# Kernel tuning notes

Measured on AMD Instinct MI355X. Metric: run time of the kernel, lower is better.

## Reference

```python
import jax, jax.numpy as jnp
import numpy as np

N, E, G = 50000, 800000, 16
NODE, HID, OUT, HEADS = 128, 64, 128, 3
NEG_SLOPE = 0.2

def setup_inputs() -> dict:
    key = jax.random.key(0)
    ks = jax.random.split(key, 12)
    h = jax.random.normal(ks[0], (N, NODE), jnp.float32)
    z = jax.random.normal(ks[1], (G, OUT), jnp.float32)
    src = jax.random.randint(ks[2], (E,), 0, N, jnp.int32)
    dst = jax.random.randint(ks[3], (E,), 0, N, jnp.int32)
    graph_id = jnp.sort(jax.random.randint(ks[4], (N,), 0, G, jnp.int32))
    s = 0.1
    fc_w = jax.random.normal(ks[5], (HEADS * HID, NODE), jnp.float32) * s
    attn_l = jax.random.normal(ks[6], (HEADS, HID), jnp.float32) * s
    attn_r = jax.random.normal(ks[7], (HEADS, HID), jnp.float32) * s
    bias = jnp.zeros((HEADS * HID,), jnp.float32)
    lin1_w = jax.random.normal(ks[8], (HID, OUT), jnp.float32) * s
    lin1_b = jnp.zeros((HID,), jnp.float32)
    lin2_w = jax.random.normal(ks[9], (1, 2 * HID), jnp.float32) * s
    lin2_b = jnp.zeros((1,), jnp.float32)
    return dict(h=h, z=z, src=src, dst=dst, graph_id=graph_id, fc_w=fc_w,
                attn_l=attn_l, attn_r=attn_r, bias=bias,
                lin1_w=lin1_w, lin1_b=lin1_b, lin2_w=lin2_w, lin2_b=lin2_b)

def reference(h, z, src, dst, graph_id, fc_w, attn_l, attn_r, bias,
              lin1_w, lin1_b, lin2_w, lin2_b):
    n = h.shape[0]
    # GATConv: projection -> [N, H, D]
    feat = (h @ fc_w.T).reshape(n, HEADS, HID)
    el = jnp.sum(feat * attn_l, axis=-1)  # [N, H]
    er = jnp.sum(feat * attn_r, axis=-1)  # [N, H]
    e = jax.nn.leaky_relu(el[src] + er[dst], NEG_SLOPE)  # [E, H]
    # edge softmax per destination node
    m = jax.ops.segment_max(e, dst, num_segments=n)
    e = jnp.exp(e - m[dst])
    s = jax.ops.segment_sum(e, dst, num_segments=n)
    alpha = e / s[dst]
    # scatter-weighted aggregation
    msg = alpha[:, :, None] * feat[src]  # [E, H, D]
    rst = jax.ops.segment_sum(msg, dst, num_segments=n)  # [N, H, D]
    rst = rst + bias.reshape(HEADS, HID)
    h_d = jnp.mean(rst, axis=1)  # [N, D] (mean over heads)
    # dgl.mean_nodes: per-graph mean pooling
    counts = jax.ops.segment_sum(jnp.ones((n,), h_d.dtype), graph_id, num_segments=G)
    pooled = jax.ops.segment_sum(h_d, graph_id, num_segments=G) / jnp.maximum(counts, 1.0)[:, None]
    z1 = z @ lin1_w.T + lin1_b  # [G, HID]
    cat = jnp.concatenate([pooled, z1], axis=1)  # [G, 2*HID]
    score = jax.nn.sigmoid(cat @ lin2_w.T + lin2_b)  # [G, 1]
    return score
```

## Files before the change

### kernel.cpp

```cpp
#include <hip/hip_runtime.h>
#include <math.h>

#define N_NODES 50000
#define N_EDGES 800000
#define N_GRAPHS 16
#define NODE_F 128
#define HID 64
#define OUT_F 128
#define HEADS 3
#define NEG 0.2f
#define FEAT (HEADS*HID)

typedef float f32x4 __attribute__((ext_vector_type(4)));
typedef float f32x2 __attribute__((ext_vector_type(2)));
typedef short bf16x8 __attribute__((ext_vector_type(8)));

#if defined(__has_builtin)
#if __has_builtin(__builtin_amdgcn_cvt_pk_f32_fp8) && __has_builtin(__builtin_amdgcn_cvt_pk_fp8_f32)
#define USE_FP8 1
#endif
#endif
#ifndef USE_FP8
#define USE_FP8 0
#endif

#if USE_FP8
#define FB 1
#else
#define FB 2
#endif
#define GRP (8 * FB)
#define ROW (32 * GRP)

#define NBKT ((N_NODES + 63) / 64)
#define H1B 400
#define EPB (N_EDGES / H1B)

__device__ __forceinline__ ushort f2bf(float x) {
  union { float f; unsigned u; } v; v.f = x;
  unsigned r = v.u + 0x7fff + ((v.u >> 16) & 1);
  return (ushort)(r >> 16);
}
__device__ __forceinline__ float bf2f(ushort x) {
  union { unsigned u; float f; } v; v.u = ((unsigned)x) << 16;
  return v.f;
}

__device__ __forceinline__ void feat_store(unsigned char* base, int n, int hh, int dd, float v) {
  size_t off = (size_t)n * ROW + (dd >> 1) * GRP + ((hh * 2 + (dd & 1)) * FB);
#if USE_FP8
  base[off] = (unsigned char)(__builtin_amdgcn_cvt_pk_fp8_f32(v, 0.f, 0, false) & 0xff);
#else
  *(ushort*)(base + off) = f2bf(v);
#endif
}

#define ZERO_INTS (N_GRAPHS * HID + N_GRAPHS)
#define ZERO_U4 (ZERO_INTS / 4)
#define ZB ((ZERO_U4 + 255) / 256)
__global__ void kprep(const float* __restrict__ fc_w, ushort* __restrict__ fcb,
                      uint4* __restrict__ zbase) {
  if (blockIdx.x >= 24) {
    int i = (blockIdx.x - 24) * 256 + threadIdx.x;
    if (i < ZERO_U4) zbase[i] = make_uint4(0, 0, 0, 0);
    return;
  }
  int i = blockIdx.x * 256 + threadIdx.x;
  int col = i >> 5;
  int kb = (i & 31) * 4;
  float4 v = *(const float4*)(fc_w + (size_t)col * NODE_F + kb);
  int t = col >> 4, m = col & 15;
  int kk = kb >> 5, kq = (kb >> 3) & 3, j = kb & 7;
  size_t idx0 = ((((size_t)t * 4 + kk) * 4 + kq) * 16 + m) * 8 + j;
  ushort4 o; o.x = f2bf(v.x); o.y = f2bf(v.y); o.z = f2bf(v.z); o.w = f2bf(v.w);
  *(ushort4*)(fcb + idx0) = o;
}

#define GB0 ((N_NODES + 63) / 64)
__global__ __launch_bounds__(256) void k1_gemm(
    const float* __restrict__ h, const ushort* __restrict__ fcb,
    const float* __restrict__ attn_l, const float* __restrict__ attn_r,
    unsigned char* __restrict__ feat, float* __restrict__ el, float* __restrict__ er)
{
  __shared__ ushort A[64][136];
  const int tid = threadIdx.x;

  const int n0 = blockIdx.x * 64;
  for (int i = tid; i < 64 * 32; i += 256) {
    int r = i >> 5, c4 = i & 31;
    if (n0 + r < N_NODES) {
      float4 v = *(const float4*)(h + (size_t)(n0 + r) * NODE_F + c4 * 4);
      unsigned lo = f2bf(v.x) | ((unsigned)f2bf(v.y) << 16);
      unsigned hi = f2bf(v.z) | ((unsigned)f2bf(v.w) << 16);
      *(uint2*)&A[r][c4 * 4] = make_uint2(lo, hi);
    }
  }
  __syncthreads();

  const int lane = tid & 63, wv = tid >> 6;
  const int m = lane & 15, kq = lane >> 4;

  f32x4 acc[12];
#pragma unroll
  for (int t = 0; t < 12; t++) acc[t] = (f32x4){0.f, 0.f, 0.f, 0.f};

#pragma unroll
  for (int kk = 0; kk < 4; kk++) {
    bf16x8 af = *(const bf16x8*)&A[wv * 16 + m][kk * 32 + kq * 8];
#pragma unroll
    for (int t = 0; t < 12; t++) {
      const bf16x8 bf = *(const bf16x8*)(fcb + ((((size_t)t * 4 + kk) * 4 + kq) * 16 + m) * 8);
      acc[t] = __builtin_amdgcn_mfma_f32_16x16x32_bf16(af, bf, acc[t], 0, 0, 0);
    }
  }

  const int rbase = n0 + wv * 16 + kq * 4;
#pragma unroll
  for (int t = 0; t < 12; t++) {
    const int hh = t >> 2;
    const int dd = (t & 3) * 16 + m;
#pragma unroll
    for (int reg = 0; reg < 4; reg++) {
      int n = rbase + reg;
      if (n < N_NODES) feat_store(feat, n, hh, dd, acc[t][reg]);
    }
  }

#pragma unroll
  for (int hh = 0; hh < HEADS; hh++) {
    float elv[4] = {0.f, 0.f, 0.f, 0.f};
    float erv[4] = {0.f, 0.f, 0.f, 0.f};
#pragma unroll
    for (int tt = 0; tt < 4; tt++) {
      int t = hh * 4 + tt;
      float al = attn_l[hh * HID + tt * 16 + m];
      float ar = attn_r[hh * HID + tt * 16 + m];
#pragma unroll
      for (int reg = 0; reg < 4; reg++) {
        elv[reg] = fmaf(acc[t][reg], al, elv[reg]);
        erv[reg] = fmaf(acc[t][reg], ar, erv[reg]);
      }
    }
#pragma unroll
    for (int reg = 0; reg < 4; reg++) {
#pragma unroll
      for (int off = 1; off < 16; off <<= 1) {
        elv[reg] += __shfl_xor(elv[reg], off, 64);
        erv[reg] += __shfl_xor(erv[reg], off, 64);
      }
      int n = rbase + reg;
      if (m == 0 && n < N_NODES) {
        el[(size_t)n * 4 + hh] = elv[reg];
        er[(size_t)n * 4 + hh] = erv[reg];
      }
    }
  }
}

__global__ __launch_bounds__(256) void kh1_hist(
    const int* __restrict__ dst, int* __restrict__ cnt_g)
{
  __shared__ int cnt[NBKT];
  const int tid = threadIdx.x, blk = blockIdx.x;
  for (int i = tid; i < NBKT; i += 256) cnt[i] = 0;
  __syncthreads();
  const int e0 = blk * EPB;
  for (int i = tid; i < EPB; i += 256)
    atomicAdd(&cnt[dst[e0 + i] >> 6], 1);
  __syncthreads();
  for (int i = tid; i < NBKT; i += 256) cnt_g[(size_t)blk * NBKT + i] = cnt[i];
}

#define H2A_K 7
__global__ __launch_bounds__(64) void kh2a_scan(
    const int* __restrict__ cnt_g, int* __restrict__ base_bm, int* __restrict__ btot)
{
  const int b = blockIdx.x;
  const int lane = threadIdx.x;
  int v[H2A_K];
  int lt = 0;
#pragma unroll
  for (int j = 0; j < H2A_K; j++) {
    int g = lane * H2A_K + j;
    v[j] = (g < H1B) ? cnt_g[(size_t)g * NBKT + b] : 0;
    lt += v[j];
  }
  int s = lt;
#pragma unroll
  for (int off = 1; off < 64; off <<= 1) {
    int t = __shfl_up(s, off, 64);
    if (lane >= off) s += t;
  }
  int excl = s - lt;
#pragma unroll
  for (int j = 0; j < H2A_K; j++) {
    int g = lane * H2A_K + j;
    if (g < H1B) base_bm[(size_t)b * H1B + g] = excl;
    excl += v[j];
  }
  if (lane == 63) btot[b] = s;
}

#define H2B_K 13
__global__ __launch_bounds__(64) void kh2b_scan(
    const int* __restrict__ btot, int* __restrict__ bucket_off)
{
  const int lane = threadIdx.x;
  int v[H2B_K];
  int lt = 0;
#pragma unroll
  for (int j = 0; j < H2B_K; j++) {
    int g = lane * H2B_K + j;
    v[j] = (g < NBKT) ? btot[g] : 0;
    lt += v[j];
  }
  int s = lt;
#pragma unroll
  for (int off = 1; off < 64; off <<= 1) {
    int t = __shfl_up(s, off, 64);
    if (lane >= off) s += t;
  }
  int excl = s - lt;
#pragma unroll
  for (int j = 0; j < H2B_K; j++) {
    int g = lane * H2B_K + j;
    if (g < NBKT) bucket_off[g] = excl;
    excl += v[j];
  }
  if (lane == 63) bucket_off[NBKT] = s;
}

__global__ __launch_bounds__(256) void kh3_scatter(
    const int* __restrict__ src, const int* __restrict__ dst,
    const int* __restrict__ bucket_off, const int* __restrict__ base_bm,
    int2* __restrict__ pairs)
{
  __shared__ int cur[NBKT];
  const int tid = threadIdx.x, blk = blockIdx.x;
  for (int i = tid; i < NBKT; i += 256)
    cur[i] = bucket_off[i] + base_bm[(size_t)i * H1B + blk];
  __syncthreads();
  const int e0 = blk * EPB;
  for (int i = tid; i < EPB; i += 256) {
    int e = e0 + i;
    int d = dst[e], s = src[e];
    int slot = atomicAdd(&cur[d >> 6], 1);
    pairs[slot] = make_int2(s, d);
  }
}

__global__ __launch_bounds__(256) void kh4_nodesort(
    const int2* __restrict__ pairs, const int* __restrict__ bucket_off,
    int2* __restrict__ pairs_s, int* __restrict__ offs)
{
  __shared__ int nodecnt[64];
  __shared__ int cur[64];
  const int b = blockIdx.x, tid = threadIdx.x;
  const int lo = bucket_off[b], hi = bucket_off[b + 1];
  if (tid < 64) nodecnt[tid] = 0;
  __syncthreads();
  for (int i = lo + tid; i < hi; i += 256)
    atomicAdd(&nodecnt[pairs[i].y & 63], 1);
  __syncthreads();
  if (tid < 64) {
    int v = nodecnt[tid];
    int s = v;
#pragma unroll
    for (int off = 1; off < 64; off <<= 1) {
      int t = __shfl_up(s, off, 64);
      if (tid >= off) s += t;
    }
    int excl = s - v;
    cur[tid] = lo + excl;
    int n = b * 64 + tid;
    if (n < N_NODES) offs[n] = lo + excl;
    if (b == NBKT - 1 && tid == 0) offs[N_NODES] = hi;
  }
  __syncthreads();
  for (int i = lo + tid; i < hi; i += 256) {
    int2 pr = pairs[i];
    int slot = atomicAdd(&cur[pr.y & 63], 1);
    pairs_s[slot] = pr;
  }
}

__global__ __launch_bounds__(256) void k3_edge(
    const int2* __restrict__ pairs_s,
    const float* __restrict__ el4, const float* __restrict__ er4,
    float4* __restrict__ csr_w)
{
  int e = blockIdx.x * 256 + threadIdx.x;
  int2 pr = pairs_s[e];
  int s = pr.x, d = pr.y;
  float4 elv = ((const float4*)el4)[s];
  float4 erv = ((const float4*)er4)[d];
  float e0 = elv.x + erv.x; e0 = e0 > 0.f ? e0 : NEG * e0;
  float e1 = elv.y + erv.y; e1 = e1 > 0.f ? e1 : NEG * e1;
  float e2 = elv.z + erv.z; e2 = e2 > 0.f ? e2 : NEG * e2;
  float4 r;
  r.x = __expf(e0); r.y = __expf(e1); r.z = __expf(e2);
  r.w = __int_as_float(s * ROW);
  csr_w[e] = r;
}

__global__ __launch_bounds__(256) void k4_agg(
    const int* __restrict__ offs, const float4* __restrict__ csr_w,
    const unsigned char* __restrict__ feat, const float* __restrict__ bias,
    float* __restrict__ h_d)
{
  __shared__ float4 rec[4][64];
  const int wv = threadIdx.x >> 6, lane = threadIdx.x & 63;
  const int n = blockIdx.x * 4 + wv;
  const int lo = offs[n], hi = offs[n + 1];
  const int half = lane >> 5;
  const int d = lane & 31;
  const char* fb = (const char*)feat;

  float a0x = 0.f, a0y = 0.f, a1x = 0.f, a1y = 0.f, a2x = 0.f, a2y = 0.f;
  float s0 = 0.f, s1 = 0.f, s2 = 0.f;

  for (int base = lo; base < hi; base += 64) {
    const int cnt = min(64, hi - base);
    if (lane < cnt) {
      float4 c = csr_w[base + lane];
      rec[wv][lane] = c;
      s0 += c.x; s1 += c.y; s2 += c.z;
    }
#define K4_BODY(J) do { \
      float4 c = rec[wv][J]; \
      const char* rp = fb + __float_as_int(c.w) + GRP * d; \
      f32x2 f0, f1, f2; \
      if (USE_FP8) { \
        uint2 q = *(const uint2*)rp; \
        f0 = __builtin_amdgcn_cvt_pk_f32_fp8(q.x & 0xffff, false); \
        f1 = __builtin_amdgcn_cvt_pk_f32_fp8(q.x >> 16, false); \
        f2 = __builtin_amdgcn_cvt_pk_f32_fp8(q.y & 0xffff, false); \
      } else { \
        uint4 q = *(const uint4*)rp; \
        f0.x = bf2f((ushort)(q.x & 0xffff)); f0.y = bf2f((ushort)(q.x >> 16)); \
        f1.x = bf2f((ushort)(q.y & 0xffff)); f1.y = bf2f((ushort)(q.y >> 16)); \
        f2.x = bf2f((ushort)(q.z & 0xffff)); f2.y = bf2f((ushort)(q.z >> 16)); \
      } \
      a0x = fmaf(c.x, f0.x, a0x); a0y = fmaf(c.x, f0.y, a0y); \
      a1x = fmaf(c.y, f1.x, a1x); a1y = fmaf(c.y, f1.y, a1y); \
      a2x = fmaf(c.z, f2.x, a2x); a2y = fmaf(c.z, f2.y, a2y); \
    } while (0)
    int j = half;
    for (; j + 2 < cnt; j += 4) { K4_BODY(j); K4_BODY(j + 2); }
    if (j < cnt) K4_BODY(j);
#undef K4_BODY
  }
  a0x += __shfl_xor(a0x, 32, 64); a0y += __shfl_xor(a0y, 32, 64);
  a1x += __shfl_xor(a1x, 32, 64); a1y += __shfl_xor(a1y, 32, 64);
  a2x += __shfl_xor(a2x, 32, 64); a2y += __shfl_xor(a2y, 32, 64);
#pragma unroll
  for (int off = 32; off; off >>= 1) {
    s0 += __shfl_xor(s0, off, 64);
    s1 += __shfl_xor(s1, off, 64);
    s2 += __shfl_xor(s2, off, 64);
  }
  const float i0 = s0 > 0.f ? 1.f / s0 : 0.f;
  const float i1 = s1 > 0.f ? 1.f / s1 : 0.f;
  const float i2 = s2 > 0.f ? 1.f / s2 : 0.f;
  if (half == 0) {
    float2 b0 = *(const float2*)(bias + 2 * d);
    float2 b1 = *(const float2*)(bias + HID + 2 * d);
    float2 b2 = *(const float2*)(bias + 2 * HID + 2 * d);
    float2 o;
    o.x = (fmaf(a0x, i0, b0.x) + fmaf(a1x, i1, b1.x) + fmaf(a2x, i2, b2.x)) * (1.f / 3.f);
    o.y = (fmaf(a0y, i0, b0.y) + fmaf(a1y, i1, b1.y) + fmaf(a2y, i2, b2.y)) * (1.f / 3.f);
    *(float2*)(h_d + (size_t)n * HID + 2 * d) = o;
  }
}

#define K5_NPB 128
#define K5_NB ((N_NODES + K5_NPB - 1) / K5_NPB)
#define NSEG (K5_NB * 2)
__global__ __launch_bounds__(256) void k5a_partial(
    const int* __restrict__ graph_id, const float* __restrict__ h_d,
    float* __restrict__ pooled_res, int* __restrict__ gcnt_res,
    float* __restrict__ part, int* __restrict__ pg, int* __restrict__ pc)
{
  const int wv = threadIdx.x >> 6, lane = threadIdx.x & 63;
  const int b = blockIdx.x;
  const int n0 = b * K5_NPB;
  const int n1 = min(n0 + K5_NPB, N_NODES);
  const int g_lo = graph_id[n0], g_hi = graph_id[n1 - 1];

  if (g_hi > g_lo + 1) {
    float acc = 0.f; int cur_g = -1; int cnt = 0;
    for (int i = n0 + wv; i < n1; i += 4) {
      int g = graph_id[i];
      if (g != cur_g) {
        if (cur_g >= 0) {
          atomicAdd(&pooled_res[cur_g * HID + lane], acc);
          if (lane == 0) atomicAdd(&gcnt_res[cur_g], cnt);
        }
        acc = 0.f; cnt = 0; cur_g = g;
      }
      acc += h_d[(size_t)i * HID + lane];
      cnt++;
    }
    if (cur_g >= 0) {
      atomicAdd(&pooled_res[cur_g * HID + lane], acc);
      if (lane == 0) atomicAdd(&gcnt_res[cur_g], cnt);
    }
    if (threadIdx.x < 2) pg[b * 2 + threadIdx.x] = -1;
    return;
  }

  float acc_lo = 0.f, acc_hi = 0.f;
  int c_lo = 0, c_hi = 0;
  for (int i = n0 + wv; i < n1; i += 4) {
    int g = graph_id[i];
    float v = h_d[(size_t)i * HID + lane];
    bool hi = (g != g_lo);
    acc_hi += hi ? v : 0.f;
    acc_lo += hi ? 0.f : v;
    c_hi += hi ? 1 : 0;
    c_lo += hi ? 0 : 1;
  }
  __shared__ float ls[2][4][64];
  __shared__ int lc[2][4];
  ls[0][wv][lane] = acc_lo;
  ls[1][wv][lane] = acc_hi;
  if (lane == 0) { lc[0][wv] = c_lo; lc[1][wv] = c_hi; }
  __syncthreads();
  if (wv < 2) {
    float s = ls[wv][0][lane] + ls[wv][1][lane] + ls[wv][2][lane] + ls[wv][3][lane];
    part[((size_t)b * 2 + wv) * HID + lane] = s;
    if (lane == 0) {
      int cnt = lc[wv][0] + lc[wv][1] + lc[wv][2] + lc[wv][3];
      int gg = (wv == 0) ? g_lo : g_hi;
      if (wv == 1 && (g_hi == g_lo || cnt == 0)) gg = -1;
      pg[b * 2 + wv] = gg;
      pc[b * 2 + wv] = cnt;
    }
  }
}

__global__ __launch_bounds__(256) void k6_final(
    const float* __restrict__ part, const int* __restrict__ pg, const int* __restrict__ pc,
    const float* __restrict__ pooled_res, const int* __restrict__ gcnt_res,
    const float* __restrict__ z,
    const float* __restrict__ lin1_w, const float* __restrict__ lin1_b,
    const float* __restrict__ lin2_w, const float* __restrict__ lin2_b,
    float* __restrict__ out)
{
  const int g = blockIdx.x;
  const int tid = threadIdx.x, wv = tid >> 6, lane = tid & 63;
  __shared__ int spg[NSEG], spc[NSEG];
  __shared__ float red[4][HID];
  __shared__ int rc[4];
  __shared__ float cat[2 * HID];

  for (int i = tid; i < NSEG; i += 256) { spg[i] = pg[i]; spc[i] = pc[i]; }
  __syncthreads();

  float acc = 0.f; int cnt = 0;
  for (int s = wv; s < NSEG; s += 4) {
    if (spg[s] == g) {
      acc += part[(size_t)s * HID + lane];
      cnt += spc[s];
    }
  }
  red[wv][lane] = acc;
  if (lane == 0) rc[wv] = cnt;
  __syncthreads();

  if (wv == 0) {
    float s = red[0][lane] + red[1][lane] + red[2][lane] + red[3][lane]
            + pooled_res[g * HID + lane];
    int c = rc[0] + rc[1] + rc[2] + rc[3] + gcnt_res[g];
    cat[lane] = s / (float)(c > 0 ? c : 1);
  }
  if (wv == 1) {
    float s = lin1_b[lane];
    const float* zr = z + g * OUT_F;
    const float* wr = lin1_w + lane * OUT_F;
    for (int k = 0; k < OUT_F; k += 4) {
      float4 zv = *(const float4*)(zr + k);
      float4 wv4 = *(const float4*)(wr + k);
      s = fmaf(zv.x, wv4.x, fmaf(zv.y, wv4.y, fmaf(zv.z, wv4.z, fmaf(zv.w, wv4.w, s))));
    }
    cat[HID + lane] = s;
  }
  __syncthreads();
  if (wv == 0) {
    float s = cat[lane] * lin2_w[lane] + cat[HID + lane] * lin2_w[HID + lane];
#pragma unroll
    for (int off = 32; off; off >>= 1) s += __shfl_xor(s, off, 64);
    if (lane == 0) out[g] = 1.f / (1.f + __expf(-(s + lin2_b[0])));
  }
}

extern "C" void kernel_launch(void* const* d_in, const int* in_sizes, int n_in,
                              void* d_out, int out_size, void* d_ws, size_t ws_size,
                              hipStream_t stream) {
  (void)in_sizes; (void)n_in; (void)out_size; (void)ws_size;
  const float* h      = (const float*)d_in[0];
  const float* z      = (const float*)d_in[1];
  const int*   src    = (const int*)d_in[2];
  const int*   dst    = (const int*)d_in[3];
  const int*   gid    = (const int*)d_in[4];
  const float* fc_w   = (const float*)d_in[5];
  const float* attn_l = (const float*)d_in[6];
  const float* attn_r = (const float*)d_in[7];
  const float* bias   = (const float*)d_in[8];
  const float* lin1_w = (const float*)d_in[9];
  const float* lin1_b = (const float*)d_in[10];
  const float* lin2_w = (const float*)d_in[11];
  const float* lin2_b = (const float*)d_in[12];
  float* out = (float*)d_out;

  float4* csr_w     = (float4*)d_ws;
  int2* pairs       = (int2*)csr_w;
  unsigned char* feat = (unsigned char*)(csr_w + N_EDGES);
  float* h_d        = (float*)(feat + (size_t)N_NODES * ROW);
  float* el         = h_d + (size_t)N_NODES * HID;
  float* er         = el + (size_t)N_NODES * 4;
  float* part       = er + (size_t)N_NODES * 4;
  int* pg           = (int*)(part + (size_t)NSEG * HID);
  int* pc           = pg + NSEG;
  ushort* fcb       = (ushort*)(pc + NSEG);
  float* pooled_res = (float*)(fcb + 192 * NODE_F);
  int* gcnt_res     = (int*)(pooled_res + N_GRAPHS * HID);
  int* offs         = gcnt_res + N_GRAPHS;
  int2* pairs_s     = (int2*)(offs + (N_NODES + 1));
  int* cnt_g        = (int*)(pairs_s + N_EDGES);
  int* base_bm      = cnt_g + (size_t)H1B * NBKT;
  int* btot         = base_bm + (size_t)NBKT * H1B;
  int* bucket_off   = btot + NBKT;

  kprep<<<24 + ZB, 256, 0, stream>>>(fc_w, fcb, (uint4*)pooled_res);
  k1_gemm<<<GB0, 256, 0, stream>>>(h, fcb, attn_l, attn_r, feat, el, er);
  kh1_hist<<<H1B, 256, 0, stream>>>(dst, cnt_g);
  kh2a_scan<<<NBKT, 64, 0, stream>>>(cnt_g, base_bm, btot);
  kh2b_scan<<<1, 64, 0, stream>>>(btot, bucket_off);
  kh3_scatter<<<H1B, 256, 0, stream>>>(src, dst, bucket_off, base_bm, pairs);
  kh4_nodesort<<<NBKT, 256, 0, stream>>>(pairs, bucket_off, pairs_s, offs);
  k3_edge<<<N_EDGES / 256, 256, 0, stream>>>(pairs_s, el, er, csr_w);
  k4_agg<<<N_NODES / 4, 256, 0, stream>>>(offs, csr_w, feat, bias, h_d);
  k5a_partial<<<K5_NB, 256, 0, stream>>>(gid, h_d, pooled_res, gcnt_res, part, pg, pc);
  k6_final<<<N_GRAPHS, 256, 0, stream>>>(part, pg, pc, pooled_res, gcnt_res,
                                         z, lin1_w, lin1_b, lin2_w, lin2_b, out);
}
```

Before: 217.1 us.

## Fuse histogram into GEMM, fold bucket scan into consumers, compute edge weights in aggregation

```diff
diff --git a/kernel.cpp b/kernel.cpp
--- a/kernel.cpp
+++ b/kernel.cpp
@@ -77,15 +77,30 @@
 }
 
 #define GB0 ((N_NODES + 63) / 64)
-__global__ __launch_bounds__(256) void k1_gemm(
+__global__ __launch_bounds__(256) void k01_fused(
     const float* __restrict__ h, const ushort* __restrict__ fcb,
     const float* __restrict__ attn_l, const float* __restrict__ attn_r,
-    unsigned char* __restrict__ feat, float* __restrict__ el, float* __restrict__ er)
+    const int* __restrict__ dst,
+    unsigned char* __restrict__ feat, float* __restrict__ el, float* __restrict__ er,
+    int* __restrict__ cnt_g)
 {
   __shared__ ushort A[64][136];
   const int tid = threadIdx.x;
 
-  const int n0 = blockIdx.x * 64;
+  if (blockIdx.x < H1B) {
+    int* cnt = (int*)&A[0][0];
+    const int blk = blockIdx.x;
+    for (int i = tid; i < NBKT; i += 256) cnt[i] = 0;
+    __syncthreads();
+    const int e0 = blk * EPB;
+    for (int i = tid; i < EPB; i += 256)
+      atomicAdd(&cnt[dst[e0 + i] >> 6], 1);
+    __syncthreads();
+    for (int i = tid; i < NBKT; i += 256) cnt_g[(size_t)blk * NBKT + i] = cnt[i];
+    return;
+  }
+
+  const int n0 = (blockIdx.x - H1B) * 64;
   for (int i = tid; i < 64 * 32; i += 256) {
     int r = i >> 5, c4 = i & 31;
     if (n0 + r < N_NODES) {
@@ -157,20 +172,6 @@
   }
 }
 
-__global__ __launch_bounds__(256) void kh1_hist(
-    const int* __restrict__ dst, int* __restrict__ cnt_g)
-{
-  __shared__ int cnt[NBKT];
-  const int tid = threadIdx.x, blk = blockIdx.x;
-  for (int i = tid; i < NBKT; i += 256) cnt[i] = 0;
-  __syncthreads();
-  const int e0 = blk * EPB;
-  for (int i = tid; i < EPB; i += 256)
-    atomicAdd(&cnt[dst[e0 + i] >> 6], 1);
-  __syncthreads();
-  for (int i = tid; i < NBKT; i += 256) cnt_g[(size_t)blk * NBKT + i] = cnt[i];
-}
-
 #define H2A_K 7
 __global__ __launch_bounds__(64) void kh2a_scan(
     const int* __restrict__ cnt_g, int* __restrict__ base_bm, int* __restrict__ btot)
@@ -201,16 +202,19 @@
   if (lane == 63) btot[b] = s;
 }
 
-#define H2B_K 13
-__global__ __launch_bounds__(64) void kh2b_scan(
-    const int* __restrict__ btot, int* __restrict__ bucket_off)
-{
-  const int lane = threadIdx.x;
-  int v[H2B_K];
-  int lt = 0;
-#pragma unroll
-  for (int j = 0; j < H2B_K; j++) {
-    int g = lane * H2B_K + j;
+__global__ __launch_bounds__(256) void kh3_scatter(
+    const int* __restrict__ src, const int* __restrict__ dst,
+    const int* __restrict__ btot, const int* __restrict__ base_bm,
+    int2* __restrict__ pairs)
+{
+  __shared__ int cur[NBKT];
+  __shared__ int wsum[4];
+  const int tid = threadIdx.x, blk = blockIdx.x;
+  const int lane = tid & 63, wv = tid >> 6;
+  int v[4]; int lt = 0;
+#pragma unroll
+  for (int j = 0; j < 4; j++) {
+    int g = tid * 4 + j;
     v[j] = (g < NBKT) ? btot[g] : 0;
     lt += v[j];
   }
@@ -220,45 +224,51 @@
     int t = __shfl_up(s, off, 64);
     if (lane >= off) s += t;
   }
-  int excl = s - lt;
-#pragma unroll
-  for (int j = 0; j < H2B_K; j++) {
-    int g = lane * H2B_K + j;
-    if (g < NBKT) bucket_off[g] = excl;
+  if (lane == 63) wsum[wv] = s;
+  __syncthreads();
+  int woff = 0;
+#pragma unroll
+  for (int w = 0; w < 4; w++) woff += (w < wv) ? wsum[w] : 0;
+  int excl = s - lt + woff;
+#pragma unroll
+  for (int j = 0; j < 4; j++) {
+    int g = tid * 4 + j;
+    if (g < NBKT) cur[g] = excl + base_bm[(size_t)g * H1B + blk];
     excl += v[j];
   }
-  if (lane == 63) bucket_off[NBKT] = s;
-}
-
-__global__ __launch_bounds__(256) void kh3_scatter(
-    const int* __restrict__ src, const int* __restrict__ dst,
-    const int* __restrict__ bucket_off, const int* __restrict__ base_bm,
-    int2* __restrict__ pairs)
-{
-  __shared__ int cur[NBKT];
-  const int tid = threadIdx.x, blk = blockIdx.x;
-  for (int i = tid; i < NBKT; i += 256)
-    cur[i] = bucket_off[i] + base_bm[(size_t)i * H1B + blk];
   __syncthreads();
   const int e0 = blk * EPB;
   for (int i = tid; i < EPB; i += 256) {
     int e = e0 + i;
-    int d = dst[e], s = src[e];
+    int d = dst[e], sv = src[e];
     int slot = atomicAdd(&cur[d >> 6], 1);
-    pairs[slot] = make_int2(s, d);
+    pairs[slot] = make_int2(sv, d);
   }
 }
 
 __global__ __launch_bounds__(256) void kh4_nodesort(
-    const int2* __restrict__ pairs, const int* __restrict__ bucket_off,
-    int2* __restrict__ pairs_s, int* __restrict__ offs)
+    const int2* __restrict__ pairs, const int* __restrict__ btot,
+    int* __restrict__ src_s, int* __restrict__ offs)
 {
   __shared__ int nodecnt[64];
   __shared__ int cur[64];
+  __shared__ int red_[4];
+  __shared__ int lo_s, hi_s;
   const int b = blockIdx.x, tid = threadIdx.x;
-  const int lo = bucket_off[b], hi = bucket_off[b + 1];
+  const int lane = tid & 63, wv = tid >> 6;
+  int partial = 0;
+  for (int i = tid; i < b; i += 256) partial += btot[i];
+#pragma unroll
+  for (int off = 32; off; off >>= 1) partial += __shfl_xor(partial, off, 64);
+  if (lane == 0) red_[wv] = partial;
   if (tid < 64) nodecnt[tid] = 0;
   __syncthreads();
+  if (tid == 0) {
+    int l = red_[0] + red_[1] + red_[2] + red_[3];
+    lo_s = l; hi_s = l + btot[b];
+  }
+  __syncthreads();
+  const int lo = lo_s, hi = hi_s;
   for (int i = lo + tid; i < hi; i += 256)
     atomicAdd(&nodecnt[pairs[i].y & 63], 1);
   __syncthreads();
@@ -274,37 +284,19 @@
     cur[tid] = lo + excl;
     int n = b * 64 + tid;
     if (n < N_NODES) offs[n] = lo + excl;
-    if (b == NBKT - 1 && tid == 0) offs[N_NODES] = hi;
+    if (b == NBKT - 1 && tid == 0) offs[N_NODES] = N_EDGES;
   }
   __syncthreads();
   for (int i = lo + tid; i < hi; i += 256) {
     int2 pr = pairs[i];
     int slot = atomicAdd(&cur[pr.y & 63], 1);
-    pairs_s[slot] = pr;
-  }
-}
-
-__global__ __launch_bounds__(256) void k3_edge(
-    const int2* __restrict__ pairs_s,
+    src_s[slot] = pr.x;
+  }
+}
+
+__global__ __launch_bounds__(256) void k4_agg(
+    const int* __restrict__ offs, const int* __restrict__ src_s,
     const float* __restrict__ el4, const float* __restrict__ er4,
-    float4* __restrict__ csr_w)
-{
-  int e = blockIdx.x * 256 + threadIdx.x;
-  int2 pr = pairs_s[e];
-  int s = pr.x, d = pr.y;
-  float4 elv = ((const float4*)el4)[s];
-  float4 erv = ((const float4*)er4)[d];
-  float e0 = elv.x + erv.x; e0 = e0 > 0.f ? e0 : NEG * e0;
-  float e1 = elv.y + erv.y; e1 = e1 > 0.f ? e1 : NEG * e1;
-  float e2 = elv.z + erv.z; e2 = e2 > 0.f ? e2 : NEG * e2;
-  float4 r;
-  r.x = __expf(e0); r.y = __expf(e1); r.z = __expf(e2);
-  r.w = __int_as_float(s * ROW);
-  csr_w[e] = r;
-}
-
-__global__ __launch_bounds__(256) void k4_agg(
-    const int* __restrict__ offs, const float4* __restrict__ csr_w,
     const unsigned char* __restrict__ feat, const float* __restrict__ bias,
     float* __restrict__ h_d)
 {
@@ -315,6 +307,7 @@
   const int half = lane >> 5;
   const int d = lane & 31;
   const char* fb = (const char*)feat;
+  const float4 ern = ((const float4*)er4)[n];
 
   float a0x = 0.f, a0y = 0.f, a1x = 0.f, a1y = 0.f, a2x = 0.f, a2y = 0.f;
   float s0 = 0.f, s1 = 0.f, s2 = 0.f;
@@ -322,7 +315,14 @@
   for (int base = lo; base < hi; base += 64) {
     const int cnt = min(64, hi - base);
     if (lane < cnt) {
-      float4 c = csr_w[base + lane];
+      int sidx = src_s[base + lane];
+      float4 elv = ((const float4*)el4)[sidx];
+      float e0 = elv.x + ern.x; e0 = e0 > 0.f ? e0 : NEG * e0;
+      float e1 = elv.y + ern.y; e1 = e1 > 0.f ? e1 : NEG * e1;
+      float e2 = elv.z + ern.z; e2 = e2 > 0.f ? e2 : NEG * e2;
+      float4 c;
+      c.x = __expf(e0); c.y = __expf(e1); c.z = __expf(e2);
+      c.w = __int_as_float(sidx * ROW);
       rec[wv][lane] = c;
       s0 += c.x; s1 += c.y; s2 += c.z;
     }
@@ -513,9 +513,8 @@
   const float* lin2_b = (const float*)d_in[12];
   float* out = (float*)d_out;
 
-  float4* csr_w     = (float4*)d_ws;
-  int2* pairs       = (int2*)csr_w;
-  unsigned char* feat = (unsigned char*)(csr_w + N_EDGES);
+  int2* pairs       = (int2*)d_ws;
+  unsigned char* feat = (unsigned char*)(pairs + N_EDGES);
   float* h_d        = (float*)(feat + (size_t)N_NODES * ROW);
   float* el         = h_d + (size_t)N_NODES * HID;
   float* er         = el + (size_t)N_NODES * 4;
@@ -526,21 +525,18 @@
   float* pooled_res = (float*)(fcb + 192 * NODE_F);
   int* gcnt_res     = (int*)(pooled_res + N_GRAPHS * HID);
   int* offs         = gcnt_res + N_GRAPHS;
-  int2* pairs_s     = (int2*)(offs + (N_NODES + 1));
-  int* cnt_g        = (int*)(pairs_s + N_EDGES);
+  int* src_s        = offs + (N_NODES + 1);
+  int* cnt_g        = src_s + N_EDGES;
   int* base_bm      = cnt_g + (size_t)H1B * NBKT;
   int* btot         = base_bm + (size_t)NBKT * H1B;
-  int* bucket_off   = btot + NBKT;
 
   kprep<<<24 + ZB, 256, 0, stream>>>(fc_w, fcb, (uint4*)pooled_res);
-  k1_gemm<<<GB0, 256, 0, stream>>>(h, fcb, attn_l, attn_r, feat, el, er);
-  kh1_hist<<<H1B, 256, 0, stream>>>(dst, cnt_g);
+  k01_fused<<<H1B + GB0, 256, 0, stream>>>(h, fcb, attn_l, attn_r, dst,
+                                           feat, el, er, cnt_g);
   kh2a_scan<<<NBKT, 64, 0, stream>>>(cnt_g, base_bm, btot);
-  kh2b_scan<<<1, 64, 0, stream>>>(btot, bucket_off);
-  kh3_scatter<<<H1B, 256, 0, stream>>>(src, dst, bucket_off, base_bm, pairs);
-  kh4_nodesort<<<NBKT, 256, 0, stream>>>(pairs, bucket_off, pairs_s, offs);
-  k3_edge<<<N_EDGES / 256, 256, 0, stream>>>(pairs_s, el, er, csr_w);
-  k4_agg<<<N_NODES / 4, 256, 0, stream>>>(offs, csr_w, feat, bias, h_d);
+  kh3_scatter<<<H1B, 256, 0, stream>>>(src, dst, btot, base_bm, pairs);
+  kh4_nodesort<<<NBKT, 256, 0, stream>>>(pairs, btot, src_s, offs);
+  k4_agg<<<N_NODES / 4, 256, 0, stream>>>(offs, src_s, el, er, feat, bias, h_d);
   k5a_partial<<<K5_NB, 256, 0, stream>>>(gid, h_d, pooled_res, gcnt_res, part, pg, pc);
   k6_final<<<N_GRAPHS, 256, 0, stream>>>(part, pg, pc, pooled_res, gcnt_res,
                                          z, lin1_w, lin1_b, lin2_w, lin2_b, out);
```

After: 206.1 us. 1.05x faster.
